# Optimization experiments

Hardware: AMD Instinct MI355X
Metric: run time of the kernel (lower is better)

## Reference

```python
import jax, jax.numpy as jnp
import numpy as np

N_NODES = 16384
N_EDGES = 32768
D = 128          # node feature / hidden dim
EDGE_DIM = 10    # bond featurizer one-hot dim
EH = 32          # edge_hidden_dim in the NNConv MLPs


def _nnconv(x, src, dst, edge_attr, l1w, l1b, l2w, l2b, root, bias):
    """PyG NNConv with aggr='mean': out_i = x_i @ root + mean_{e: dst=i} x_{src_e} @ W(e) + bias."""
    E = edge_attr.shape[0]
    h = jax.nn.relu(edge_attr @ l1w + l1b)              # [E, EH]
    W = (h @ l2w + l2b).reshape(E, D, D)                # per-edge weight matrices [E, D, D]
    msg = jnp.einsum('ei,eio->eo', x[src], W)           # gather + per-edge matmul [E, D]
    s = jax.ops.segment_sum(msg, dst, num_segments=N_NODES)
    cnt = jax.ops.segment_sum(jnp.ones((E, 1), x.dtype), dst, num_segments=N_NODES)
    agg = s / jnp.maximum(cnt, 1.0)                     # scatter-mean (0 for isolated nodes)
    return x @ root + agg + bias


def setup_inputs() -> dict:
    key = jax.random.key(0)
    ks = jax.random.split(key, 14)
    x = jax.random.normal(ks[0], (N_NODES, D), dtype=jnp.float32)
    edge_index = jax.random.randint(ks[1], (2, N_EDGES), 0, N_NODES, dtype=jnp.int64)
    edge_attr = jax.random.uniform(ks[2], (N_EDGES, EDGE_DIM), dtype=jnp.float32)

    def lin(k, fan_in, fan_out):
        return jax.random.normal(k, (fan_in, fan_out), dtype=jnp.float32) / np.sqrt(fan_in)

    return {
        'x': x, 'edge_index': edge_index, 'edge_attr': edge_attr,
        # subgraph_conv1 (128 -> 128)
        'w1_l1': lin(ks[3], EDGE_DIM, EH), 'b1_l1': jnp.zeros((EH,), jnp.float32),
        'w1_l2': lin(ks[4], EH, D * D),    'b1_l2': jnp.zeros((D * D,), jnp.float32),
        'w1_root': lin(ks[5], D, D),       'b1': jnp.zeros((D,), jnp.float32),
        # subgraph_conv2 (128 -> 128), applied twice with shared weights
        'w2_l1': lin(ks[6], EDGE_DIM, EH), 'b2_l1': jnp.zeros((EH,), jnp.float32),
        'w2_l2': lin(ks[7], EH, D * D),    'b2_l2': jnp.zeros((D * D,), jnp.float32),
        'w2_root': lin(ks[8], D, D),       'b2': jnp.zeros((D,), jnp.float32),
    }


def reference(x, edge_index, edge_attr,
              w1_l1, b1_l1, w1_l2, b1_l2, w1_root, b1,
              w2_l1, b2_l1, w2_l2, b2_l2, w2_root, b2):
    src, dst = edge_index[0], edge_index[1]
    h = jax.nn.relu(_nnconv(x, src, dst, edge_attr, w1_l1, b1_l1, w1_l2, b1_l2, w1_root, b1))
    h = jax.nn.relu(_nnconv(h, src, dst, edge_attr, w2_l1, b2_l1, w2_l2, b2_l2, w2_root, b2))
    h = _nnconv(h, src, dst, edge_attr, w2_l1, b2_l1, w2_l2, b2_l2, w2_root, b2)
    return h
```

## Files before the change

### kernel.cpp

```cpp
#include <hip/hip_runtime.h>

#define N_NODES 16384
#define N_EDGES 32768
#define D 128
#define EDGE_DIM 10
#define KH 32
#define BM 64
#define XST2 72
#define XST 136
#define NBL 32

typedef _Float16 f16;
typedef _Float16 f16x4 __attribute__((ext_vector_type(4)));
typedef _Float16 f16x8 __attribute__((ext_vector_type(8)));
typedef float f32x4 __attribute__((ext_vector_type(4)));

__global__ __launch_bounds__(256) void deg_pack_kernel(
    const int* __restrict__ ei, int* __restrict__ deg,
    const float* __restrict__ w1l2, const float* __restrict__ w2l2,
    const float* __restrict__ b1l2, const float* __restrict__ b2l2,
    const float* __restrict__ rt1, const float* __restrict__ rt2,
    f16* __restrict__ Bp1, f16* __restrict__ Bp2,
    f16* __restrict__ Rp1, f16* __restrict__ Rp2) {
  int y = blockIdx.y;
  if (y == 0) {
    int e = blockIdx.x * 256 + threadIdx.x;
    if (e < N_EDGES) atomicAdd(&deg[ei[N_EDGES + e]], 1);
    return;
  }
  if (blockIdx.x >= D * D / 256) return;
  int t = blockIdx.x * 256 + threadIdx.x;
  int j = y - 1;
  if (j < 2) {
    const float* l2w = j ? w2l2 : w1l2;
    f16* Bp = j ? Bp2 : Bp1;
    f16 tmp[KH];
#pragma unroll
    for (int k = 0; k < KH; k++) tmp[k] = (f16)l2w[(size_t)k * (D * D) + t];
    f16x8* dst = (f16x8*)(Bp + (size_t)t * KH);
#pragma unroll
    for (int c = 0; c < 4; c++) dst[c] = *(f16x8*)&tmp[c * 8];
  } else {
    const float* src = (j == 2) ? b1l2 : (j == 3) ? b2l2 : (j == 4) ? rt1 : rt2;
    f16* dst = (j == 2) ? (Bp1 + (size_t)D * D * KH)
             : (j == 3) ? (Bp2 + (size_t)D * D * KH)
             : (j == 4) ? Rp1 : Rp2;
    int i = t >> 7, o = t & 127;
    dst[((size_t)(i >> 5) * D + o) * KH + (i & 31)] = (f16)src[t];
  }
}

__global__ __launch_bounds__(1024) void scan_kernel(
    const int* __restrict__ deg, int* __restrict__ rs, int* __restrict__ fill) {
  __shared__ int part[1024];
  int t = threadIdx.x;
  int base = t * 16;
  int loc[16], s = 0;
#pragma unroll
  for (int j = 0; j < 16; j++) { loc[j] = deg[base + j]; s += loc[j]; }
  part[t] = s;
  __syncthreads();
  for (int off = 1; off < 1024; off <<= 1) {
    int add = (t >= off) ? part[t - off] : 0;
    __syncthreads();
    part[t] += add;
    __syncthreads();
  }
  int run = t ? part[t - 1] : 0;
#pragma unroll
  for (int j = 0; j < 16; j++) {
    rs[base + j] = run; fill[base + j] = run; run += loc[j];
  }
  if (t == 1023) rs[N_NODES] = run;
}

__global__ __launch_bounds__(256) void scatter_kernel(
    const int* __restrict__ ei, int* __restrict__ fill,
    int* __restrict__ perm, int* __restrict__ srcs) {
  int e = blockIdx.x * blockDim.x + threadIdx.x;
  if (e < N_EDGES) {
    int pos = atomicAdd(&fill[ei[N_EDGES + e]], 1);
    perm[pos] = e;
    srcs[pos] = ei[e];
  }
}

__global__ __launch_bounds__(256) void edge_mlp_kernel(
    const float* __restrict__ ea, const int* __restrict__ perm,
    const float* __restrict__ w1l1, const float* __restrict__ b1l1,
    const float* __restrict__ w2l1, const float* __restrict__ b2l1,
    f16* __restrict__ h1, f16* __restrict__ h2) {
  int p = blockIdx.x * blockDim.x + threadIdx.x;
  const float* l1w = blockIdx.y ? w2l1 : w1l1;
  const float* l1b = blockIdx.y ? b2l1 : b1l1;
  f16* h = blockIdx.y ? h2 : h1;
  int e = perm[p];
  float a[EDGE_DIM];
#pragma unroll
  for (int d = 0; d < EDGE_DIM; d++) a[d] = ea[e * EDGE_DIM + d];
  f16 hv[KH];
#pragma unroll
  for (int k = 0; k < KH; k++) {
    float acc = l1b[k];
#pragma unroll
    for (int d = 0; d < EDGE_DIM; d++) acc += a[d] * l1w[d * KH + k];
    hv[k] = (f16)fmaxf(acc, 0.0f);
  }
  f16x8* dst = (f16x8*)(h + (size_t)p * KH);
#pragma unroll
  for (int c = 0; c < 4; c++) dst[c] = *(f16x8*)&hv[c * 8];
}

__global__ __launch_bounds__(256, 4) void msg_mfma_kernel(
    const float* __restrict__ xin, const f16* __restrict__ hf,
    const f16* __restrict__ Bp, const int* __restrict__ srcs,
    f16* __restrict__ msgfA, f16* __restrict__ msgfB) {
  __shared__ f16 Xs[BM][XST2];
  __shared__ f16 Hs[BM][KH];
  int t = threadIdx.x;
  int e0 = blockIdx.x * BM;
  int y  = blockIdx.y;
  f16* msgf = y ? msgfB : msgfA;

  ((f16x8*)Hs)[t] = ((const f16x8*)(hf + (size_t)e0 * KH))[t];
  {
    int r = t >> 2, q = t & 3;
    int s = srcs[e0 + r];
    const float4* src = (const float4*)(xin + (size_t)s * D + y * 64 + q * 16);
    f16* dst = &Xs[r][q * 16];
#pragma unroll
    for (int c = 0; c < 4; c++) {
      float4 v = src[c];
      f16x4 h4 = {(f16)v.x, (f16)v.y, (f16)v.z, (f16)v.w};
      *(f16x4*)(dst + c * 4) = h4;
    }
  }

  int L = t & 63, w = t >> 6;
  int quad = L >> 4, lm = L & 15;
  int n0 = w * 32;

  const f16* bl = Bp + ((size_t)(y * 64) * D + n0 + lm) * KH + quad * 8;
  const size_t istr = (size_t)D * KH;

  f32x4 acc[4][2];
#pragma unroll
  for (int mt = 0; mt < 4; mt++)
#pragma unroll
    for (int nt = 0; nt < 2; nt++)
      acc[mt][nt] = (f32x4){0.f, 0.f, 0.f, 0.f};

  f16x8 bufA[4][2], bufB[4][2];

  auto loadg = [&](f16x8 (&buf)[4][2], int basei) {
#pragma unroll
    for (int jj = 0; jj < 4; jj++) {
      const f16* bi = bl + (size_t)(basei + jj) * istr;
      buf[jj][0] = *(const f16x8*)bi;
      buf[jj][1] = *(const f16x8*)(bi + 16 * KH);
    }
  };

  f16x8 hreg[4];

  auto compute = [&](f16x8 (&buf)[4][2], int ig) {
    f16x4 xv[4];
#pragma unroll
    for (int mt = 0; mt < 4; mt++)
      xv[mt] = *(const f16x4*)&Xs[mt * 16 + lm][ig];
#pragma unroll
    for (int jj = 0; jj < 4; jj++) {
#pragma unroll
      for (int mt = 0; mt < 4; mt++) {
        f16 xs = xv[mt][jj];
        f16x8 xb = {xs, xs, xs, xs, xs, xs, xs, xs};
        f16x8 a = hreg[mt] * xb;
        acc[mt][0] = __builtin_amdgcn_mfma_f32_16x16x32_f16(a, buf[jj][0], acc[mt][0], 0, 0, 0);
        acc[mt][1] = __builtin_amdgcn_mfma_f32_16x16x32_f16(a, buf[jj][1], acc[mt][1], 0, 0, 0);
      }
    }
  };

  loadg(bufA, 0);
  __syncthreads();

#pragma unroll
  for (int mt = 0; mt < 4; mt++)
    hreg[mt] = *(const f16x8*)&Hs[mt * 16 + lm][quad * 8];

#pragma unroll 1
  for (int g = 0; g < 8; g++) {
    loadg(bufB, 8 * g + 4);
    compute(bufA, 8 * g);
    loadg(bufA, 8 * g + 8);
    compute(bufB, 8 * g + 4);
  }

  {
    const f16* bb = Bp + (size_t)D * D * KH;
#pragma unroll
    for (int g2 = 0; g2 < 2; g2++) {
      int ig2 = 2 * y + g2;
      const f16* b2l = bb + ((size_t)ig2 * D + n0 + lm) * KH + quad * 8;
      f16x8 b0 = *(const f16x8*)b2l;
      f16x8 b1 = *(const f16x8*)(b2l + 16 * KH);
      int lc = g2 * 32 + quad * 8;
#pragma unroll
      for (int mt = 0; mt < 4; mt++) {
        f16x8 a = *(const f16x8*)&Xs[mt * 16 + lm][lc];
        acc[mt][0] = __builtin_amdgcn_mfma_f32_16x16x32_f16(a, b0, acc[mt][0], 0, 0, 0);
        acc[mt][1] = __builtin_amdgcn_mfma_f32_16x16x32_f16(a, b1, acc[mt][1], 0, 0, 0);
      }
    }
  }

#pragma unroll
  for (int mt = 0; mt < 4; mt++)
#pragma unroll
    for (int r = 0; r < 4; r++) {
      f16* mg = msgf + (size_t)(e0 + mt * 16 + quad * 4 + r) * D + n0 + lm;
      mg[0]  = (f16)acc[mt][0][r];
      mg[16] = (f16)acc[mt][1][r];
    }
}

__global__ __launch_bounds__(256) void node_update_kernel(
    const float* __restrict__ xin, const f16* __restrict__ msgA,
    const f16* __restrict__ msgB, const int* __restrict__ rs,
    const f16* __restrict__ Rp, const float* __restrict__ bias,
    float* __restrict__ out, int do_relu) {
  __shared__ f16 Xs[NBL][XST];
  __shared__ float Sls[NBL][D];
  int t = threadIdx.x;
  int nb = blockIdx.x * NBL;

  {
    int r = t >> 3, q = t & 7;
    const float4* src = (const float4*)(xin + (size_t)(nb + r) * D + q * 16);
    f16* dst = &Xs[r][q * 16];
#pragma unroll
    for (int c = 0; c < 4; c++) {
      float4 v = src[c];
      f16x4 h4 = {(f16)v.x, (f16)v.y, (f16)v.z, (f16)v.w};
      *(f16x4*)(dst + c * 4) = h4;
    }
  }
  __syncthreads();

  {
    int nl = t >> 3, o0 = (t & 7) * 16;
    int n = nb + nl;
    int a = rs[n], b = rs[n + 1];
    float sum[16];
#pragma unroll
    for (int j = 0; j < 16; j++) sum[j] = 0.f;
    for (int r = a; r < b; r++) {
      f16x8 a0 = *(const f16x8*)(msgA + (size_t)r * D + o0);
      f16x8 a1 = *(const f16x8*)(msgA + (size_t)r * D + o0 + 8);
      f16x8 b0 = *(const f16x8*)(msgB + (size_t)r * D + o0);
      f16x8 b1 = *(const f16x8*)(msgB + (size_t)r * D + o0 + 8);
#pragma unroll
      for (int j = 0; j < 8; j++) {
        sum[j]     += (float)a0[j] + (float)b0[j];
        sum[8 + j] += (float)a1[j] + (float)b1[j];
      }
    }
    float inv = 1.0f / (float)max(b - a, 1);
#pragma unroll
    for (int j = 0; j < 16; j++) Sls[nl][o0 + j] = sum[j] * inv;
  }
  __syncthreads();

  int L = t & 63, w = t >> 6;
  int quad = L >> 4, lm = L & 15;
  int n0 = w * 32;
  f32x4 acc[2][2];
#pragma unroll
  for (int mt = 0; mt < 2; mt++)
#pragma unroll
    for (int nt = 0; nt < 2; nt++)
      acc[mt][nt] = (f32x4){0.f, 0.f, 0.f, 0.f};
#pragma unroll
  for (int s4 = 0; s4 < 4; s4++) {
    const f16* b2l = Rp + ((size_t)s4 * D + n0 + lm) * KH + quad * 8;
    f16x8 b0 = *(const f16x8*)b2l;
    f16x8 b1 = *(const f16x8*)(b2l + 16 * KH);
#pragma unroll
    for (int mt = 0; mt < 2; mt++) {
      f16x8 a = *(const f16x8*)&Xs[mt * 16 + lm][s4 * 32 + quad * 8];
      acc[mt][0] = __builtin_amdgcn_mfma_f32_16x16x32_f16(a, b0, acc[mt][0], 0, 0, 0);
      acc[mt][1] = __builtin_amdgcn_mfma_f32_16x16x32_f16(a, b1, acc[mt][1], 0, 0, 0);
    }
  }
#pragma unroll
  for (int mt = 0; mt < 2; mt++)
#pragma unroll
    for (int r = 0; r < 4; r++) {
      Sls[mt * 16 + quad * 4 + r][n0 + lm] += acc[mt][0][r];
      Sls[mt * 16 + quad * 4 + r][n0 + 16 + lm] += acc[mt][1][r];
    }
  __syncthreads();

  {
    int o = t & 127, g = t >> 7;
    float bo = bias[o];
    for (int q = g * 16; q < g * 16 + 16; q++) {
      float v = bo + Sls[q][o];
      out[(size_t)(nb + q) * D + o] = do_relu ? fmaxf(v, 0.0f) : v;
    }
  }
}

extern "C" void kernel_launch(void* const* d_in, const int* in_sizes, int n_in,
                              void* d_out, int out_size, void* d_ws, size_t ws_size,
                              hipStream_t stream) {
  const float* x      = (const float*)d_in[0];
  const int*   ei     = (const int*)d_in[1];
  const float* ea     = (const float*)d_in[2];
  const float* w1_l1  = (const float*)d_in[3];
  const float* b1_l1  = (const float*)d_in[4];
  const float* w1_l2  = (const float*)d_in[5];
  const float* b1_l2  = (const float*)d_in[6];
  const float* w1_rt  = (const float*)d_in[7];
  const float* b1     = (const float*)d_in[8];
  const float* w2_l1  = (const float*)d_in[9];
  const float* b2_l1  = (const float*)d_in[10];
  const float* w2_l2  = (const float*)d_in[11];
  const float* b2_l2  = (const float*)d_in[12];
  const float* w2_rt  = (const float*)d_in[13];
  const float* b2     = (const float*)d_in[14];
  float* out = (float*)d_out;

  const size_t BPSZ = (size_t)D * D * KH + (size_t)D * D + 32768;
  f16* h1f = (f16*)d_ws;
  f16* h2f = h1f + (size_t)N_EDGES * KH;
  f16* Bp1 = h2f + (size_t)N_EDGES * KH;
  f16* Bp2 = Bp1 + BPSZ;
  f16* Rp1 = Bp2 + BPSZ;
  f16* Rp2 = Rp1 + (size_t)D * D;
  int* deg  = (int*)(Rp2 + (size_t)D * D);
  int* rs   = deg + N_NODES;
  int* fill = rs + N_NODES + 128;
  int* perm = fill + N_NODES;
  int* srcs = perm + N_EDGES;
  f16* msgA = (f16*)(srcs + N_EDGES);
  f16* msgB = msgA + (size_t)N_EDGES * D;

  hipMemsetAsync(deg, 0, N_NODES * sizeof(int), stream);
  deg_pack_kernel<<<dim3(N_EDGES / 256, 7), 256, 0, stream>>>(
      ei, deg, w1_l2, w2_l2, b1_l2, b2_l2, w1_rt, w2_rt, Bp1, Bp2, Rp1, Rp2);
  scan_kernel<<<1, 1024, 0, stream>>>(deg, rs, fill);
  scatter_kernel<<<N_EDGES / 256, 256, 0, stream>>>(ei, fill, perm, srcs);
  edge_mlp_kernel<<<dim3(N_EDGES / 256, 2), 256, 0, stream>>>(
      ea, perm, w1_l1, b1_l1, w2_l1, b2_l1, h1f, h2f);

  msg_mfma_kernel<<<dim3(N_EDGES / BM, 2), 256, 0, stream>>>(x, h1f, Bp1, srcs, msgA, msgB);
  node_update_kernel<<<N_NODES / NBL, 256, 0, stream>>>(x, msgA, msgB, rs, Rp1, b1, out, 1);
  msg_mfma_kernel<<<dim3(N_EDGES / BM, 2), 256, 0, stream>>>(out, h2f, Bp2, srcs, msgA, msgB);
  node_update_kernel<<<N_NODES / NBL, 256, 0, stream>>>(out, msgA, msgB, rs, Rp2, b2, out, 1);
  msg_mfma_kernel<<<dim3(N_EDGES / BM, 2), 256, 0, stream>>>(out, h2f, Bp2, srcs, msgA, msgB);
  node_update_kernel<<<N_NODES / NBL, 256, 0, stream>>>(out, msgA, msgB, rs, Rp2, b2, out, 0);
}
```

Baseline: 260.2 us.

## Use inline-asm global loads with explicit vmcnt waits for deeper B prefetch

Replaces the compiler-scheduled B-fragment loads in the message MFMA kernel with inline-asm global_load_dwordx4 and manual s_waitcnt vmcnt(8)/vmcnt(0) plus sched barriers. Both buffers are kept in flight so each compute phase overlaps the next group's loads. The loop also stops loading past the end, which the old version did on its final iteration. Launch bounds are relaxed from 4 to 2 blocks per SIMD to give more registers, at the cost of occupancy. The hand-placed waits assume the compiler emits no other vector memory ops in between.

```diff
diff --git a/kernel.cpp b/kernel.cpp
--- a/kernel.cpp
+++ b/kernel.cpp
@@ -14,6 +14,10 @@
 typedef _Float16 f16x4 __attribute__((ext_vector_type(4)));
 typedef _Float16 f16x8 __attribute__((ext_vector_type(8)));
 typedef float f32x4 __attribute__((ext_vector_type(4)));
+
+__device__ __forceinline__ void ld16(f16x8 &d, const f16* p) {
+  asm volatile("global_load_dwordx4 %0, %1, off" : "=v"(d) : "v"(p) : "memory");
+}
 
 __global__ __launch_bounds__(256) void deg_pack_kernel(
     const int* __restrict__ ei, int* __restrict__ deg,
@@ -111,7 +115,7 @@
   for (int c = 0; c < 4; c++) dst[c] = *(f16x8*)&hv[c * 8];
 }
 
-__global__ __launch_bounds__(256, 4) void msg_mfma_kernel(
+__global__ __launch_bounds__(256, 2) void msg_mfma_kernel(
     const float* __restrict__ xin, const f16* __restrict__ hf,
     const f16* __restrict__ Bp, const int* __restrict__ srcs,
     f16* __restrict__ msgfA, f16* __restrict__ msgfB) {
@@ -152,13 +156,22 @@
 
   f16x8 bufA[4][2], bufB[4][2];
 
-  auto loadg = [&](f16x8 (&buf)[4][2], int basei) {
+  auto issueB = [&](f16x8 (&buf)[4][2], int basei) {
 #pragma unroll
     for (int jj = 0; jj < 4; jj++) {
       const f16* bi = bl + (size_t)(basei + jj) * istr;
-      buf[jj][0] = *(const f16x8*)bi;
-      buf[jj][1] = *(const f16x8*)(bi + 16 * KH);
-    }
+      ld16(buf[jj][0], bi);
+      ld16(buf[jj][1], bi + 16 * KH);
+    }
+  };
+
+  auto wait8 = [&]() {
+    asm volatile("s_waitcnt vmcnt(8)" ::: "memory");
+    __builtin_amdgcn_sched_barrier(0);
+  };
+  auto wait0 = [&]() {
+    asm volatile("s_waitcnt vmcnt(0)" ::: "memory");
+    __builtin_amdgcn_sched_barrier(0);
   };
 
   f16x8 hreg[4];
@@ -181,20 +194,28 @@
     }
   };
 
-  loadg(bufA, 0);
   __syncthreads();
 
 #pragma unroll
   for (int mt = 0; mt < 4; mt++)
     hreg[mt] = *(const f16x8*)&Hs[mt * 16 + lm][quad * 8];
 
+  issueB(bufA, 0);
+  issueB(bufB, 4);
+
 #pragma unroll 1
-  for (int g = 0; g < 8; g++) {
-    loadg(bufB, 8 * g + 4);
-    compute(bufA, 8 * g);
-    loadg(bufA, 8 * g + 8);
-    compute(bufB, 8 * g + 4);
-  }
+  for (int gi = 0; gi < 7; gi++) {
+    wait8();
+    compute(bufA, 8 * gi);
+    issueB(bufA, 8 * gi + 8);
+    wait8();
+    compute(bufB, 8 * gi + 4);
+    issueB(bufB, 8 * gi + 12);
+  }
+  wait8();
+  compute(bufA, 56);
+  wait0();
+  compute(bufB, 60);
 
   {
     const f16* bb = Bp + (size_t)D * D * KH;
```

Result: no change. 257.2 us (-1.2%).
